# Kernel tuning notes

Measured on AMD Instinct MI355X. Metric: run time of the kernel, lower is better.

The kernel has to match this reference:

```python
import jax, jax.numpy as jnp
import numpy as np

N_NODES = 50000
N_EDGES = 1600000
D = 128


def setup_inputs() -> dict:
    key = jax.random.key(0)
    k1, k2, k3, k4 = jax.random.split(key, 4)
    x = jax.random.normal(k1, (N_NODES, D), dtype=jnp.float32)
    edge_index = jax.random.randint(k2, (2, N_EDGES), 0, N_NODES, dtype=jnp.int64)
    # Xavier-uniform-like W; B is zeros in torch init but use small random for grad coverage
    limit = float(np.sqrt(6.0 / (D + D)))
    W = jax.random.uniform(k3, (D, D), dtype=jnp.float32, minval=-limit, maxval=limit)
    B = jax.random.uniform(k4, (D, D), dtype=jnp.float32, minval=-limit, maxval=limit)
    return {"x": x, "edge_index": edge_index, "W": W, "B": B}


def reference(x, edge_index, W, B):
    sources = edge_index[0]
    destinations = edge_index[1]
    # gather messages from source nodes, scatter-add into destinations
    messages = x[sources]  # [E, D]
    aggregated = jax.ops.segment_sum(messages, destinations, num_segments=N_NODES)  # [N, D]
    deg = jax.ops.segment_sum(jnp.ones((N_EDGES,), dtype=x.dtype), destinations, num_segments=N_NODES)
    deg = jnp.where(deg == 0, jnp.asarray(1.0, dtype=x.dtype), deg)
    mean_msg = aggregated / deg[:, None]
    # update: messages @ W.T + x @ B.T
    return mean_msg @ W.T + x @ B.T
```

## Files before the change

### kernel.cpp

```cpp
#include <hip/hip_runtime.h>
#include <hip/hip_bf16.h>

#define NN 50000
#define NE 1600000
#define DD 128
#define NPB 64
#define NBK 782
#define MAXB 2560
#define CHUNK 6144
#define NCB 261
#define WSM 136

typedef __attribute__((ext_vector_type(8))) short short8;
typedef __attribute__((ext_vector_type(4))) float f32x4;

__device__ inline unsigned short to_bf16(float v) {
    __hip_bfloat16 h = __float2bfloat16(v);
    return __builtin_bit_cast(unsigned short, h);
}

__global__ __launch_bounds__(1024) void convscatter_k(const int* __restrict__ ei,
                                                      const float* __restrict__ x,
                                                      const float* __restrict__ W,
                                                      const float* __restrict__ Bm,
                                                      unsigned int* __restrict__ xb,
                                                      unsigned short* __restrict__ Wbf,
                                                      unsigned short* __restrict__ Bbf,
                                                      int* __restrict__ gcursor,
                                                      int* __restrict__ ebuf) {
    __shared__ int stg[CHUNK];
    __shared__ int h[NBK];
    __shared__ int lbase[NBK];
    __shared__ int gb[NBK];
    __shared__ int hcur[NBK];
    __shared__ int wsum[16], wbase[16];
    const int t = threadIdx.x;
    const int lane = t & 63, wv = t >> 6;
    const int e0 = blockIdx.x * CHUNK;
    const int ec = min(CHUNK, NE - e0);

    for (int i = t; i < NBK; i += 1024) h[i] = 0;
    __syncthreads();

    unsigned int w2[6];
    #pragma unroll
    for (int u = 0; u < 6; ++u) {
        int i = u * 1024 + t;
        if (i < ec) {
            int src = ei[e0 + i];
            int dst = ei[NE + e0 + i];
            int b = dst >> 6;
            w2[u] = ((unsigned)b << 22) | ((unsigned)src << 6) | (unsigned)(dst & 63);
            atomicAdd(&h[b], 1);
        } else w2[u] = 0xFFFFFFFFu;
    }

    {
        int gid = blockIdx.x * 1024 + t;
        const int total4 = NN * DD / 4;
        for (int i = gid; i < total4; i += NCB * 1024) {
            float4 v = ((const float4*)x)[i];
            int p = __builtin_amdgcn_cvt_pk_fp8_f32(v.x, v.y, 0, false);
            p = __builtin_amdgcn_cvt_pk_fp8_f32(v.z, v.w, p, true);
            xb[i] = (unsigned)p;
        }
    }
    if (blockIdx.x == NCB - 1) {
        for (int i = t; i < DD * DD / 4; i += 1024) {
            float4 w4 = ((const float4*)W)[i];
            float4 b4 = ((const float4*)Bm)[i];
            ushort4 wp, bp;
            wp.x = to_bf16(w4.x); wp.y = to_bf16(w4.y); wp.z = to_bf16(w4.z); wp.w = to_bf16(w4.w);
            bp.x = to_bf16(b4.x); bp.y = to_bf16(b4.y); bp.z = to_bf16(b4.z); bp.w = to_bf16(b4.w);
            ((ushort4*)Wbf)[i] = wp;
            ((ushort4*)Bbf)[i] = bp;
        }
    }
    __syncthreads();

    int v = (t < NBK) ? h[t] : 0;
    int s = v;
    #pragma unroll
    for (int o = 1; o < 64; o <<= 1) {
        int u = __shfl_up(s, o);
        if (lane >= o) s += u;
    }
    if (lane == 63) wsum[wv] = s;
    __syncthreads();
    if (wv == 0 && lane < 16) {
        int bv = wsum[lane];
        int bs = bv;
        #pragma unroll
        for (int o = 1; o < 16; o <<= 1) {
            int u = __shfl_up(bs, o);
            if (lane >= o) bs += u;
        }
        wbase[lane] = bs - bv;
    }
    __syncthreads();
    if (t < NBK) {
        int excl = s - v + wbase[wv];
        lbase[t] = excl;
        hcur[t] = excl;
        gb[t] = v ? t * MAXB + atomicAdd(&gcursor[t], v) : 0;
    }
    __syncthreads();

    #pragma unroll
    for (int u = 0; u < 6; ++u) {
        if (w2[u] != 0xFFFFFFFFu) {
            int b = w2[u] >> 22;
            int pos = atomicAdd(&hcur[b], 1);
            stg[pos] = (int)w2[u];
        }
    }
    __syncthreads();

    for (int i = t; i < ec; i += 1024) {
        unsigned int w = (unsigned)stg[i];
        int b = w >> 22;
        ebuf[gb[b] + (i - lbase[b])] = (int)(w & 0x3FFFFFu);
    }
}

#define ACC2(U)                                                              \
    {                                                                        \
        auto l0 = __builtin_amdgcn_cvt_pk_f32_fp8((int)(U).x, false);        \
        auto h0 = __builtin_amdgcn_cvt_pk_f32_fp8((int)(U).x, true);         \
        auto l1 = __builtin_amdgcn_cvt_pk_f32_fp8((int)(U).y, false);        \
        auto h1 = __builtin_amdgcn_cvt_pk_f32_fp8((int)(U).y, true);         \
        a0 += l0[0]; a1 += l0[1]; a2 += h0[0]; a3 += h0[1];                  \
        a4 += l1[0]; a5 += l1[1]; a6 += h1[0]; a7 += h1[1];                  \
    }

__global__ __launch_bounds__(512) void fused_k(const unsigned int* __restrict__ xb,
                                               const int* __restrict__ ebuf,
                                               const int* __restrict__ gcursor,
                                               const unsigned short* __restrict__ Wbf,
                                               const unsigned short* __restrict__ Bbf,
                                               const float* __restrict__ x,
                                               float* __restrict__ out) {
    __shared__ int stg[MAXB];
    __shared__ unsigned short srt[MAXB];
    __shared__ int cnt8[8][NPB];
    __shared__ int cur[NPB], off[NPB + 1];
    __shared__ unsigned short meanL[NPB * WSM];
    const int b = blockIdx.x, t = threadIdx.x;
    const int wv = t >> 6, lane = t & 63;
    const int n = min(gcursor[b], MAXB);
    const int* __restrict__ slab = ebuf + (size_t)b * MAXB;

    cnt8[wv][lane] = 0;
    for (int i = t; i < n; i += 512) {
        int v = slab[i];
        stg[i] = v;
        atomicAdd(&cnt8[wv][v & 63], 1);
    }
    __syncthreads();
    if (t < 64) {
        int v = 0;
        #pragma unroll
        for (int w = 0; w < 8; ++w) v += cnt8[w][t];
        int s = v;
        #pragma unroll
        for (int o = 1; o < 64; o <<= 1) {
            int u = __shfl_up(s, o);
            if (t >= o) s += u;
        }
        cur[t] = s - v;
        off[t] = s - v;
        if (t == 63) off[64] = s;
    }
    __syncthreads();
    for (int i = t; i < n; i += 512) {
        int w = stg[i];
        int pos = atomicAdd(&cur[w & 63], 1);
        srt[pos] = (unsigned short)(w >> 6);
    }
    __syncthreads();

    const int sub = lane >> 4, il2 = lane & 15;
    #pragma unroll
    for (int q = 0; q < 8; ++q) {
        int ln = wv + q * 8;
        int s0 = off[ln], s1 = off[ln + 1];
        float a0 = 0.f, a1 = 0.f, a2 = 0.f, a3 = 0.f;
        float a4 = 0.f, a5 = 0.f, a6 = 0.f, a7 = 0.f;
        int i = s0;
        for (; i + 32 <= s1; i += 32) {
            uint2 u[8];
            #pragma unroll
            for (int k = 0; k < 8; ++k)
                u[k] = ((const uint2*)xb)[(size_t)srt[i + 4 * k + sub] * 16 + il2];
            #pragma unroll
            for (int k = 0; k < 8; ++k) ACC2(u[k]);
        }
        if (i + 16 <= s1) {
            uint2 u[4];
            #pragma unroll
            for (int k = 0; k < 4; ++k)
                u[k] = ((const uint2*)xb)[(size_t)srt[i + 4 * k + sub] * 16 + il2];
            #pragma unroll
            for (int k = 0; k < 4; ++k) ACC2(u[k]);
            i += 16;
        }
        for (; i < s1; i += 4) {
            int e = i + sub;
            uint2 u;
            if (e < s1) u = ((const uint2*)xb)[(size_t)srt[e] * 16 + il2];
            else { u.x = 0u; u.y = 0u; }
            ACC2(u);
        }
        a0 += __shfl_xor(a0, 16); a0 += __shfl_xor(a0, 32);
        a1 += __shfl_xor(a1, 16); a1 += __shfl_xor(a1, 32);
        a2 += __shfl_xor(a2, 16); a2 += __shfl_xor(a2, 32);
        a3 += __shfl_xor(a3, 16); a3 += __shfl_xor(a3, 32);
        a4 += __shfl_xor(a4, 16); a4 += __shfl_xor(a4, 32);
        a5 += __shfl_xor(a5, 16); a5 += __shfl_xor(a5, 32);
        a6 += __shfl_xor(a6, 16); a6 += __shfl_xor(a6, 32);
        a7 += __shfl_xor(a7, 16); a7 += __shfl_xor(a7, 32);
        float inv = 1.0f / fmaxf((float)(s1 - s0), 1.0f);
        if (lane < 16) {
            short8 sv;
            sv[0] = (short)to_bf16(a0 * inv); sv[1] = (short)to_bf16(a1 * inv);
            sv[2] = (short)to_bf16(a2 * inv); sv[3] = (short)to_bf16(a3 * inv);
            sv[4] = (short)to_bf16(a4 * inv); sv[5] = (short)to_bf16(a5 * inv);
            sv[6] = (short)to_bf16(a6 * inv); sv[7] = (short)to_bf16(a7 * inv);
            *(short8*)&meanL[ln * WSM + il2 * 8] = sv;
        }
    }
    __syncthreads();

    const int rt = wv >> 1, ch = wv & 1;
    const int m = lane & 15, quad = lane >> 4;
    const int rowA = min(b * 64 + rt * 16 + m, NN - 1);

    short8 xh[4], xl[4];
    #pragma unroll
    for (int tt = 0; tt < 4; ++tt) {
        int k8 = tt * 32 + quad * 8;
        const float4* xq = (const float4*)&x[(size_t)rowA * DD + k8];
        float4 b0 = xq[0], b1 = xq[1];
        float xv[8];
        xv[0] = b0.x; xv[1] = b0.y; xv[2] = b0.z; xv[3] = b0.w;
        xv[4] = b1.x; xv[5] = b1.y; xv[6] = b1.z; xv[7] = b1.w;
        #pragma unroll
        for (int j = 0; j < 8; ++j) {
            unsigned short g = to_bf16(xv[j]);
            xh[tt][j] = (short)g;
            xl[tt][j] = (short)to_bf16(xv[j] - __uint_as_float((unsigned)g << 16));
        }
    }

    f32x4 acc[4];
    #pragma unroll
    for (int nt = 0; nt < 4; ++nt) acc[nt] = (f32x4){0.f, 0.f, 0.f, 0.f};

    #pragma unroll
    for (int tt = 0; tt < 4; ++tt) {
        int k8 = tt * 32 + quad * 8;
        short8 mf = *(const short8*)&meanL[(rt * 16 + m) * WSM + k8];
        #pragma unroll
        for (int nt = 0; nt < 4; ++nt) {
            int nrow = ch * 64 + nt * 16 + m;
            short8 wf = *(const short8*)&Wbf[(size_t)nrow * DD + k8];
            short8 bf = *(const short8*)&Bbf[(size_t)nrow * DD + k8];
            acc[nt] = __builtin_amdgcn_mfma_f32_16x16x32_bf16(xl[tt], bf, acc[nt], 0, 0, 0);
            acc[nt] = __builtin_amdgcn_mfma_f32_16x16x32_bf16(mf, wf, acc[nt], 0, 0, 0);
            acc[nt] = __builtin_amdgcn_mfma_f32_16x16x32_bf16(xh[tt], bf, acc[nt], 0, 0, 0);
        }
    }

    const int rowD0 = b * 64 + rt * 16 + quad * 4;
    #pragma unroll
    for (int nt = 0; nt < 4; ++nt) {
        #pragma unroll
        for (int r = 0; r < 4; ++r) {
            int row = rowD0 + r;
            if (row < NN) out[(size_t)row * DD + ch * 64 + nt * 16 + m] = acc[nt][r];
        }
    }
}

extern "C" void kernel_launch(void* const* d_in, const int* in_sizes, int n_in,
                              void* d_out, int out_size, void* d_ws, size_t ws_size,
                              hipStream_t stream) {
    const float* x  = (const float*)d_in[0];
    const int*   ei = (const int*)d_in[1];
    const float* W  = (const float*)d_in[2];
    const float* Bm = (const float*)d_in[3];
    float* out = (float*)d_out;

    unsigned int* xb     = (unsigned int*)d_ws;
    int* ebuf            = (int*)(xb + (size_t)NN * 32);
    unsigned short* Wbf  = (unsigned short*)(ebuf + (size_t)NBK * MAXB);
    unsigned short* Bbf  = Wbf + DD * DD;
    int* gcursor         = (int*)(Bbf + DD * DD);

    hipMemsetAsync(gcursor, 0, NBK * sizeof(int), stream);
    convscatter_k<<<NCB, 1024, 0, stream>>>(ei, x, W, Bm, xb, Wbf, Bbf, gcursor, ebuf);
    fused_k<<<NBK, 512, 0, stream>>>(xb, ebuf, gcursor, Wbf, Bbf, x, out);
}
```

Measured before the change: 173.6 us.

## Split fused aggregate+GEMM into half-slab sort-aggregate and separate MFMA GEMM kernels

Aggregation now runs twice as many blocks, each sorting and summing half of a bucket's edge slab. Partial sums and counts are written to global memory, and a new GEMM kernel combines the two halves, computes the mean and runs the bf16 MFMA with W/B staged in LDS. The conversion/scatter kernel also uses smaller chunks with more blocks. The aim is more parallelism and occupancy in the gather phase; the cost is an extra kernel launch and roughly 50MB of fp32 partial-sum round-trip traffic.

```diff
diff --git a/kernel.cpp b/kernel.cpp
--- a/kernel.cpp
+++ b/kernel.cpp
@@ -7,9 +7,10 @@
 #define NPB 64
 #define NBK 782
 #define MAXB 2560
-#define CHUNK 6144
-#define NCB 261
-#define WSM 136
+#define HSLAB 1280
+#define CHUNK 3072
+#define NCB 521
+#define WS 136
 
 typedef __attribute__((ext_vector_type(8))) short short8;
 typedef __attribute__((ext_vector_type(4))) float f32x4;
@@ -42,9 +43,9 @@
     for (int i = t; i < NBK; i += 1024) h[i] = 0;
     __syncthreads();
 
-    unsigned int w2[6];
-    #pragma unroll
-    for (int u = 0; u < 6; ++u) {
+    unsigned int w2[3];
+    #pragma unroll
+    for (int u = 0; u < 3; ++u) {
         int i = u * 1024 + t;
         if (i < ec) {
             int src = ei[e0 + i];
@@ -107,7 +108,7 @@
     __syncthreads();
 
     #pragma unroll
-    for (int u = 0; u < 6; ++u) {
+    for (int u = 0; u < 3; ++u) {
         if (w2[u] != 0xFFFFFFFFu) {
             int b = w2[u] >> 22;
             int pos = atomicAdd(&hcur[b], 1);
@@ -133,25 +134,27 @@
         a4 += l1[0]; a5 += l1[1]; a6 += h1[0]; a7 += h1[1];                  \
     }
 
-__global__ __launch_bounds__(512) void fused_k(const unsigned int* __restrict__ xb,
-                                               const int* __restrict__ ebuf,
-                                               const int* __restrict__ gcursor,
-                                               const unsigned short* __restrict__ Wbf,
-                                               const unsigned short* __restrict__ Bbf,
-                                               const float* __restrict__ x,
-                                               float* __restrict__ out) {
-    __shared__ int stg[MAXB];
-    __shared__ unsigned short srt[MAXB];
+__global__ __launch_bounds__(512) void sortagg_k(const unsigned int* __restrict__ xb,
+                                                 const int* __restrict__ ebuf,
+                                                 const int* __restrict__ gcursor,
+                                                 float* __restrict__ psum,
+                                                 unsigned short* __restrict__ pcnt) {
+    __shared__ int stg[HSLAB];
+    __shared__ unsigned short srt[HSLAB];
     __shared__ int cnt8[8][NPB];
     __shared__ int cur[NPB], off[NPB + 1];
-    __shared__ unsigned short meanL[NPB * WSM];
-    const int b = blockIdx.x, t = threadIdx.x;
+    const int blk = blockIdx.x;
+    const int b = blk >> 1, hb = blk & 1;
+    const int t = threadIdx.x;
     const int wv = t >> 6, lane = t & 63;
     const int n = min(gcursor[b], MAXB);
-    const int* __restrict__ slab = ebuf + (size_t)b * MAXB;
+    const int mid = n >> 1;
+    const int g0 = hb ? mid : 0, g1 = hb ? n : mid;
+    const int len = g1 - g0;
+    const int* __restrict__ slab = ebuf + (size_t)b * MAXB + g0;
 
     cnt8[wv][lane] = 0;
-    for (int i = t; i < n; i += 512) {
+    for (int i = t; i < len; i += 512) {
         int v = slab[i];
         stg[i] = v;
         atomicAdd(&cnt8[wv][v & 63], 1);
@@ -172,7 +175,7 @@
         if (t == 63) off[64] = s;
     }
     __syncthreads();
-    for (int i = t; i < n; i += 512) {
+    for (int i = t; i < len; i += 512) {
         int w = stg[i];
         int pos = atomicAdd(&cur[w & 63], 1);
         srt[pos] = (unsigned short)(w >> 6);
@@ -187,29 +190,24 @@
         float a0 = 0.f, a1 = 0.f, a2 = 0.f, a3 = 0.f;
         float a4 = 0.f, a5 = 0.f, a6 = 0.f, a7 = 0.f;
         int i = s0;
-        for (; i + 32 <= s1; i += 32) {
-            uint2 u[8];
-            #pragma unroll
-            for (int k = 0; k < 8; ++k)
-                u[k] = ((const uint2*)xb)[(size_t)srt[i + 4 * k + sub] * 16 + il2];
-            #pragma unroll
-            for (int k = 0; k < 8; ++k) ACC2(u[k]);
-        }
-        if (i + 16 <= s1) {
+        for (; i + 16 <= s1; i += 16) {
             uint2 u[4];
             #pragma unroll
             for (int k = 0; k < 4; ++k)
                 u[k] = ((const uint2*)xb)[(size_t)srt[i + 4 * k + sub] * 16 + il2];
             #pragma unroll
             for (int k = 0; k < 4; ++k) ACC2(u[k]);
-            i += 16;
-        }
-        for (; i < s1; i += 4) {
-            int e = i + sub;
-            uint2 u;
-            if (e < s1) u = ((const uint2*)xb)[(size_t)srt[e] * 16 + il2];
-            else { u.x = 0u; u.y = 0u; }
-            ACC2(u);
+        }
+        if (i < s1) {
+            uint2 u[4];
+            #pragma unroll
+            for (int k = 0; k < 4; ++k) {
+                int e = i + 4 * k + sub;
+                if (e < s1) u[k] = ((const uint2*)xb)[(size_t)srt[e] * 16 + il2];
+                else { u[k].x = 0u; u[k].y = 0u; }
+            }
+            #pragma unroll
+            for (int k = 0; k < 4; ++k) ACC2(u[k]);
         }
         a0 += __shfl_xor(a0, 16); a0 += __shfl_xor(a0, 32);
         a1 += __shfl_xor(a1, 16); a1 += __shfl_xor(a1, 32);
@@ -219,65 +217,99 @@
         a5 += __shfl_xor(a5, 16); a5 += __shfl_xor(a5, 32);
         a6 += __shfl_xor(a6, 16); a6 += __shfl_xor(a6, 32);
         a7 += __shfl_xor(a7, 16); a7 += __shfl_xor(a7, 32);
-        float inv = 1.0f / fmaxf((float)(s1 - s0), 1.0f);
-        if (lane < 16) {
-            short8 sv;
-            sv[0] = (short)to_bf16(a0 * inv); sv[1] = (short)to_bf16(a1 * inv);
-            sv[2] = (short)to_bf16(a2 * inv); sv[3] = (short)to_bf16(a3 * inv);
-            sv[4] = (short)to_bf16(a4 * inv); sv[5] = (short)to_bf16(a5 * inv);
-            sv[6] = (short)to_bf16(a6 * inv); sv[7] = (short)to_bf16(a7 * inv);
-            *(short8*)&meanL[ln * WSM + il2 * 8] = sv;
-        }
-    }
-    __syncthreads();
-
-    const int rt = wv >> 1, ch = wv & 1;
-    const int m = lane & 15, quad = lane >> 4;
-    const int rowA = min(b * 64 + rt * 16 + m, NN - 1);
-
-    short8 xh[4], xl[4];
-    #pragma unroll
-    for (int tt = 0; tt < 4; ++tt) {
-        int k8 = tt * 32 + quad * 8;
-        const float4* xq = (const float4*)&x[(size_t)rowA * DD + k8];
-        float4 b0 = xq[0], b1 = xq[1];
+        int node = b * NPB + ln;
+        if (node < NN) {
+            if (lane < 16) {
+                float4* P = (float4*)&psum[((size_t)hb * NN + node) * DD + il2 * 8];
+                P[0] = make_float4(a0, a1, a2, a3);
+                P[1] = make_float4(a4, a5, a6, a7);
+            }
+            if (lane == 0) pcnt[hb * NN + node] = (unsigned short)(s1 - s0);
+        }
+    }
+}
+
+__global__ __launch_bounds__(256) void gemm_mfma_k(const float* __restrict__ psum,
+                                                   const unsigned short* __restrict__ pcnt,
+                                                   const float* __restrict__ x,
+                                                   const unsigned short* __restrict__ Wbf,
+                                                   const unsigned short* __restrict__ Bbf,
+                                                   float* __restrict__ out) {
+    __shared__ unsigned short Wt[DD * WS];
+    __shared__ unsigned short Bt[DD * WS];
+    const int tid = threadIdx.x;
+    #pragma unroll
+    for (int it = 0; it < 16; ++it) {
+        int idx = it * 256 + tid;
+        int n = idx >> 5;
+        int k0 = (idx & 31) * 4;
+        *(ushort4*)&Wt[n * WS + k0] = ((const ushort4*)Wbf)[idx];
+        *(ushort4*)&Bt[n * WS + k0] = ((const ushort4*)Bbf)[idx];
+    }
+    __syncthreads();
+
+    const int wave = tid >> 6;
+    const int lane = tid & 63;
+    const int m = lane & 15;
+    const int quad = lane >> 4;
+    const int rowA = min(blockIdx.x * 64 + wave * 16 + m, NN - 1);
+
+    const float deg = (float)(pcnt[rowA] + pcnt[NN + rowA]);
+    const float inv = 1.0f / fmaxf(deg, 1.0f);
+    const float4* P0 = (const float4*)&psum[(size_t)rowA * DD];
+    const float4* P1 = (const float4*)&psum[((size_t)NN + rowA) * DD];
+
+    f32x4 acc[8];
+    #pragma unroll
+    for (int nt = 0; nt < 8; ++nt) acc[nt] = (f32x4){0.f, 0.f, 0.f, 0.f};
+
+    #pragma unroll
+    for (int t = 0; t < 4; ++t) {
+        const int k8 = t * 32 + quad * 8;
+        float4 sa = P0[k8 / 4], sb = P0[k8 / 4 + 1];
+        float4 ua = P1[k8 / 4], ub = P1[k8 / 4 + 1];
+        short8 mf;
+        mf[0] = (short)to_bf16((sa.x + ua.x) * inv);
+        mf[1] = (short)to_bf16((sa.y + ua.y) * inv);
+        mf[2] = (short)to_bf16((sa.z + ua.z) * inv);
+        mf[3] = (short)to_bf16((sa.w + ua.w) * inv);
+        mf[4] = (short)to_bf16((sb.x + ub.x) * inv);
+        mf[5] = (short)to_bf16((sb.y + ub.y) * inv);
+        mf[6] = (short)to_bf16((sb.z + ub.z) * inv);
+        mf[7] = (short)to_bf16((sb.w + ub.w) * inv);
+
         float xv[8];
-        xv[0] = b0.x; xv[1] = b0.y; xv[2] = b0.z; xv[3] = b0.w;
-        xv[4] = b1.x; xv[5] = b1.y; xv[6] = b1.z; xv[7] = b1.w;
+        {
+            const float4* xq = (const float4*)&x[(size_t)rowA * DD + k8];
+            float4 b0 = xq[0], b1 = xq[1];
+            xv[0] = b0.x; xv[1] = b0.y; xv[2] = b0.z; xv[3] = b0.w;
+            xv[4] = b1.x; xv[5] = b1.y; xv[6] = b1.z; xv[7] = b1.w;
+        }
+        short8 xh, xl;
         #pragma unroll
         for (int j = 0; j < 8; ++j) {
             unsigned short g = to_bf16(xv[j]);
-            xh[tt][j] = (short)g;
-            xl[tt][j] = (short)to_bf16(xv[j] - __uint_as_float((unsigned)g << 16));
-        }
-    }
-
-    f32x4 acc[4];
-    #pragma unroll
-    for (int nt = 0; nt < 4; ++nt) acc[nt] = (f32x4){0.f, 0.f, 0.f, 0.f};
-
-    #pragma unroll
-    for (int tt = 0; tt < 4; ++tt) {
-        int k8 = tt * 32 + quad * 8;
-        short8 mf = *(const short8*)&meanL[(rt * 16 + m) * WSM + k8];
-        #pragma unroll
-        for (int nt = 0; nt < 4; ++nt) {
-            int nrow = ch * 64 + nt * 16 + m;
-            short8 wf = *(const short8*)&Wbf[(size_t)nrow * DD + k8];
-            short8 bf = *(const short8*)&Bbf[(size_t)nrow * DD + k8];
-            acc[nt] = __builtin_amdgcn_mfma_f32_16x16x32_bf16(xl[tt], bf, acc[nt], 0, 0, 0);
+            xh[j] = (short)g;
+            xl[j] = (short)to_bf16(xv[j] - __uint_as_float((unsigned)g << 16));
+        }
+        #pragma unroll
+        for (int nt = 0; nt < 8; ++nt) {
+            int nrow = nt * 16 + m;
+            short8 wf = *(const short8*)&Wt[nrow * WS + k8];
+            short8 bf = *(const short8*)&Bt[nrow * WS + k8];
+            acc[nt] = __builtin_amdgcn_mfma_f32_16x16x32_bf16(xl, bf, acc[nt], 0, 0, 0);
             acc[nt] = __builtin_amdgcn_mfma_f32_16x16x32_bf16(mf, wf, acc[nt], 0, 0, 0);
-            acc[nt] = __builtin_amdgcn_mfma_f32_16x16x32_bf16(xh[tt], bf, acc[nt], 0, 0, 0);
-        }
-    }
-
-    const int rowD0 = b * 64 + rt * 16 + quad * 4;
-    #pragma unroll
-    for (int nt = 0; nt < 4; ++nt) {
+            acc[nt] = __builtin_amdgcn_mfma_f32_16x16x32_bf16(xh, bf, acc[nt], 0, 0, 0);
+        }
+    }
+
+    const int rowD0 = blockIdx.x * 64 + wave * 16 + quad * 4;
+    #pragma unroll
+    for (int nt = 0; nt < 8; ++nt) {
         #pragma unroll
         for (int r = 0; r < 4; ++r) {
             int row = rowD0 + r;
-            if (row < NN) out[(size_t)row * DD + ch * 64 + nt * 16 + m] = acc[nt][r];
+            if (row < NN) out[(size_t)row * DD + nt * 16 + m] = acc[nt][r];
         }
     }
 }
@@ -291,13 +323,16 @@
     const float* Bm = (const float*)d_in[3];
     float* out = (float*)d_out;
 
-    unsigned int* xb     = (unsigned int*)d_ws;
+    float* psum          = (float*)d_ws;
+    unsigned int* xb     = (unsigned int*)(psum + 2 * (size_t)NN * DD);
     int* ebuf            = (int*)(xb + (size_t)NN * 32);
     unsigned short* Wbf  = (unsigned short*)(ebuf + (size_t)NBK * MAXB);
     unsigned short* Bbf  = Wbf + DD * DD;
-    int* gcursor         = (int*)(Bbf + DD * DD);
+    unsigned short* pcnt = Bbf + DD * DD;
+    int* gcursor         = (int*)(pcnt + 2 * (size_t)NN);
 
     hipMemsetAsync(gcursor, 0, NBK * sizeof(int), stream);
     convscatter_k<<<NCB, 1024, 0, stream>>>(ei, x, W, Bm, xb, Wbf, Bbf, gcursor, ebuf);
-    fused_k<<<NBK, 512, 0, stream>>>(xb, ebuf, gcursor, Wbf, Bbf, x, out);
-}
+    sortagg_k<<<NBK * 2, 512, 0, stream>>>(xb, ebuf, gcursor, psum, pcnt);
+    gemm_mfma_k<<<(NN + 63) / 64, 256, 0, stream>>>(psum, pcnt, x, Wbf, Bbf, out);
+}
```

New measurement: 161.1 us. 7.2% less time.
